# Optimization experiments

Hardware: AMD Instinct MI355X
Metric: run time of the kernel (lower is better)

The kernel has to match this reference:

```python
import jax, jax.numpy as jnp
import numpy as np

N_MEMORY = 128
INPUT_LEN = 512
OUTPUT_LEN = 256
N_FRAMES = 65536


def setup_inputs() -> dict:
    key = jax.random.key(0)
    k1, k2, k3, k4, k5 = jax.random.split(key, 5)
    return {
        "inputs": jax.random.normal(k1, (INPUT_LEN, N_FRAMES), dtype=jnp.float32),
        "W1": jax.random.normal(k2, (2 * N_MEMORY, INPUT_LEN), dtype=jnp.float32) * 0.05,
        "B1": jax.random.normal(k3, (2 * N_MEMORY, 1), dtype=jnp.float32) * 0.05,
        "W2": jax.random.normal(k4, (OUTPUT_LEN, N_MEMORY), dtype=jnp.float32) * 0.05,
        "B2": jax.random.normal(k5, (OUTPUT_LEN, 1), dtype=jnp.float32) * 0.05,
    }


def reference(inputs, W1, B1, W2, B2):
    # h: (2M, T)
    h = jax.nn.sigmoid(jnp.matmul(W1, inputs) + B1)
    M = W1.shape[0] // 2
    left, right = h[:M], h[M:]          # each (M, T)
    prod = left * right                  # gate product, (M, T)

    # Linear recurrence: u_0 = 0; u_t = prod[:, t-1] * u_{t-1} + (1 - left[:, t-1])
    # Affine pairs for t = 1..T-1, time-major: (T-1, M)
    a = prod[:, :-1].T
    b = (1.0 - left[:, :-1]).T

    def combine(c1, c2):
        a1, b1 = c1
        a2, b2 = c2
        return a1 * a2, a2 * b1 + b2

    _, bb = jax.lax.associative_scan(combine, (a, b))
    # u_0 = 0 => u_t = bb_t; prepend the zero initial state as column 0
    z = jnp.concatenate([jnp.zeros((M, 1), dtype=inputs.dtype), bb.T], axis=1)  # (M, T)

    out = 1.0 - jax.nn.sigmoid(jnp.matmul(W2, z) + B2)  # (output_len, T)
    return out
```

## Files before the change

### kernel.cpp

```cpp
#include <hip/hip_runtime.h>

typedef unsigned short u16;
typedef short bf16x8 __attribute__((ext_vector_type(8)));
typedef float f32x4 __attribute__((ext_vector_type(4)));

#define NF 65536
#define NSC 1024
#define NMAC 16

__device__ __forceinline__ float sigm(float x){ return 1.0f/(1.0f+__expf(-x)); }

__device__ __forceinline__ u16 f2bf(float f){
  union { float f; unsigned u; } v; v.f = f;
  unsigned r = (v.u + 0x7fffu + ((v.u >> 16) & 1u)) >> 16;
  return (u16)r;
}

#define AS1(p) ((const __attribute__((address_space(1))) unsigned int*)(p))
#define AS3(p) ((__attribute__((address_space(3))) unsigned int*)(p))

__global__ __launch_bounds__(256) void k_prep(const float* __restrict__ W1, const float* __restrict__ W2,
                                              u16* __restrict__ W1f, u16* __restrict__ W2f){
  int idx = blockIdx.x*256 + threadIdx.x;
  {
    int j  = idx & 7;
    int L  = (idx >> 3) & 63;
    int ks = (idx >> 9) & 1;
    int rt = (idx >> 10) & 15;
    int ck = idx >> 14;
    int row = 16*rt + (L & 15);
    int k   = ck*64 + ks*32 + ((L >> 4) << 3) + j;
    W1f[idx] = f2bf(W1[row*512 + k]);
  }
  if (idx < 32768){
    int j  = idx & 7;
    int L  = (idx >> 3) & 63;
    int ks = (idx >> 9) & 3;
    int rt = idx >> 11;
    int row = 16*rt + (L & 15);
    int m   = ks*32 + ((L >> 4) << 3) + j;
    W2f[idx] = f2bf(W2[row*128 + m]);
  }
}

__global__ __launch_bounds__(256, 4) void k_gemm1(const float* __restrict__ x,
        const u16* __restrict__ W1f, const float* __restrict__ B1,
        float* __restrict__ Aa, float* __restrict__ Bb,
        float* __restrict__ Ac, float* __restrict__ Bc){
  __shared__ __align__(16) float ls[8192];
  __shared__ __align__(16) u16  xs[4096];
  const int tid = threadIdx.x;
  const int wv = tid >> 6, L = tid & 63;
  const int q = L >> 4, ln = L & 15;
  const int g = blockIdx.x;
  const int F0 = g * 64;
  const int rt0 = 2*wv;
  const bf16x8* W1f8 = (const bf16x8*)W1f;

  f32x4 acc[4][4];
  #pragma unroll
  for (int a=0;a<4;a++)
    #pragma unroll
    for (int c=0;c<4;c++) acc[a][c] = (f32x4){0.f,0.f,0.f,0.f};

  #pragma unroll
  for (int i=0;i<4;i++){
    int seg = wv*4 + i;
    __builtin_amdgcn_global_load_lds(
      AS1(x + (size_t)(seg*4 + q)*NF + F0 + ln*4),
      AS3(ls + seg*256), 16, 0, 0);
  }

  for (int ck=0; ck<8; ++ck){
    __syncthreads();
    if (ck < 7){
      #pragma unroll
      for (int i=0;i<4;i++){
        int seg = wv*4 + i;
        __builtin_amdgcn_global_load_lds(
          AS1(x + (size_t)((ck+1)*64 + seg*4 + q)*NF + F0 + ln*4),
          AS3(ls + ((ck+1)&1)*4096 + seg*256), 16, 0, 0);
      }
    }
    bf16x8 af[2][4];
    #pragma unroll
    for (int ks=0;ks<2;ks++){
      af[ks][0] = W1f8[ck*2048 + ((rt0  )*2+ks)*64 + L];
      af[ks][1] = W1f8[ck*2048 + ((rt0+1)*2+ks)*64 + L];
      af[ks][2] = W1f8[ck*2048 + ((rt0+8)*2+ks)*64 + L];
      af[ks][3] = W1f8[ck*2048 + ((rt0+9)*2+ks)*64 + L];
    }
    {
      const float* lsb = ls + (ck&1)*4096;
      #pragma unroll
      for (int i=0;i<2;i++){
        int s    = tid + 256*i;
        int lns  = s & 15;
        int cc   = (s >> 4) & 3;
        int qs   = (s >> 6) & 3;
        int kss  = (s >> 8) & 1;
        const float* rp = lsb + (kss*32 + qs*8)*64 + cc*16 + lns;
        unsigned u[8];
        #pragma unroll
        for (int j=0;j<8;j++) u[j] = f2bf(rp[j*64]);
        uint4 pk;
        pk.x = u[0] | (u[1]<<16); pk.y = u[2] | (u[3]<<16);
        pk.z = u[4] | (u[5]<<16); pk.w = u[6] | (u[7]<<16);
        *(uint4*)(xs + ((cc*2+kss)*64 + qs*16 + lns)*8) = pk;
      }
    }
    __syncthreads();
    #pragma unroll
    for (int ks=0; ks<2; ++ks){
      #pragma unroll
      for (int c=0;c<4;c++){
        bf16x8 bf = ((const bf16x8*)xs)[(c*2+ks)*64 + L];
        acc[0][c] = __builtin_amdgcn_mfma_f32_16x16x32_bf16(af[ks][0], bf, acc[0][c], 0,0,0);
        acc[1][c] = __builtin_amdgcn_mfma_f32_16x16x32_bf16(af[ks][1], bf, acc[1][c], 0,0,0);
        acc[2][c] = __builtin_amdgcn_mfma_f32_16x16x32_bf16(af[ks][2], bf, acc[2][c], 0,0,0);
        acc[3][c] = __builtin_amdgcn_mfma_f32_16x16x32_bf16(af[ks][3], bf, acc[3][c], 0,0,0);
      }
    }
  }

  float bl[2][4], br[2][4], RA[2][4], RB[2][4];
  #pragma unroll
  for (int pr=0;pr<2;pr++){
    int mb = 32*wv + 16*pr + 4*q;
    #pragma unroll
    for (int r=0;r<4;r++){ bl[pr][r] = B1[mb+r]; br[pr][r] = B1[mb+128+r]; }
  }
  #pragma unroll
  for (int c=0;c<4;c++){
    int t = F0 + 16*c + ln;
    #pragma unroll
    for (int pr=0;pr<2;pr++){
      int mb = 32*wv + 16*pr + 4*q;
      f32x4 Lv = acc[pr][c], Rv = acc[pr+2][c];
      float a4[4], b4[4];
      #pragma unroll
      for (int r=0;r<4;r++){
        float le = sigm(Lv[r] + bl[pr][r]);
        float ri = sigm(Rv[r] + br[pr][r]);
        a4[r] = le*ri; b4[r] = 1.0f - le;
      }
      *(float4*)(Aa + (size_t)t*128 + mb) = make_float4(a4[0],a4[1],a4[2],a4[3]);
      *(float4*)(Bb + (size_t)t*128 + mb) = make_float4(b4[0],b4[1],b4[2],b4[3]);
      #pragma unroll
      for (int r=0;r<4;r++){
        float As = a4[r], Bs = b4[r];
        #pragma unroll
        for (int d=1; d<16; d<<=1){
          float Ap = __shfl_xor(As, d);
          float Bp = __shfl_xor(Bs, d);
          Bs = (ln & d) ? fmaf(As, Bp, Bs) : fmaf(Ap, Bs, Bp);
          As *= Ap;
        }
        if (c == 0){ RA[pr][r] = As; RB[pr][r] = Bs; }
        else       { RB[pr][r] = fmaf(As, RB[pr][r], Bs); RA[pr][r] *= As; }
      }
    }
  }
  if (ln == 0){
    #pragma unroll
    for (int pr=0;pr<2;pr++){
      int mb = 32*wv + 16*pr + 4*q;
      #pragma unroll
      for (int r=0;r<4;r++){
        Ac[g*128 + mb + r] = RA[pr][r];
        Bc[g*128 + mb + r] = RB[pr][r];
      }
    }
  }
}

__global__ __launch_bounds__(256) void k_scan(const float* __restrict__ Ac, const float* __restrict__ Bc,
                                              float* __restrict__ MtA, float* __restrict__ MtB){
  __shared__ float sA[2][128], sB[2][128];
  const int j = blockIdx.x;
  const int m = threadIdx.x & 127, s4 = threadIdx.x >> 7;
  const int c0 = j*64 + s4*32;
  float A = 1.f, B = 0.f;
  #pragma unroll 8
  for (int i=0;i<32;i++){
    float a = Ac[(c0+i)*128 + m], b = Bc[(c0+i)*128 + m];
    B = fmaf(a, B, b);
    A *= a;
  }
  sA[s4][m] = A; sB[s4][m] = B;
  __syncthreads();
  if (s4 == 0){
    MtA[j*128+m] = sA[1][m] * sA[0][m];
    MtB[j*128+m] = fmaf(sA[1][m], sB[0][m], sB[1][m]);
  }
}

__global__ __launch_bounds__(256, 4) void k_apply(const float* __restrict__ Aa, const float* __restrict__ Bb,
        const float* __restrict__ Ac, const float* __restrict__ Bc,
        const float* __restrict__ MtA, const float* __restrict__ MtB,
        const u16* __restrict__ W2f, const float* __restrict__ B2,
        float* __restrict__ out){
  __shared__ __align__(16) u16 zf[8192];
  __shared__ float sA[2][128], sB[2][128];
  const int tid = threadIdx.x;
  const int g = blockIdx.x, T0 = g*64;
  const int m = tid & 127, s4 = tid >> 7;

  float vg;
  {
    const int j = g >> 6, r0 = j << 6, n = g & 63;
    int c0 = r0 + s4*32, c1 = r0 + n; if (c1 > c0+32) c1 = c0+32;
    float A = 1.f, B = 0.f;
    for (int c = c0; c < c1; ++c){
      float a = Ac[c*128 + m], b = Bc[c*128 + m];
      B = fmaf(a, B, b);
      A *= a;
    }
    sA[s4][m] = A; sB[s4][m] = B;
    float v = 0.f;
    for (int jj=0; jj<j; ++jj) v = fmaf(MtA[jj*128+m], v, MtB[jj*128+m]);
    __syncthreads();
    v = fmaf(sA[0][m], v, sB[0][m]);
    v = fmaf(sA[1][m], v, sB[1][m]);
    vg = v;
    __syncthreads();
  }

  {
    const float* ap = Aa + (size_t)(T0 + s4*32)*128 + m;
    const float* bp = Bb + (size_t)(T0 + s4*32)*128 + m;
    float areg[32], breg[32];
    #pragma unroll
    for (int i=0;i<32;i++){ areg[i] = ap[(size_t)i*128]; breg[i] = bp[(size_t)i*128]; }
    float A = 1.f, Bv = 0.f;
    #pragma unroll
    for (int i=0;i<32;i++){ Bv = fmaf(areg[i], Bv, breg[i]); A *= areg[i]; }
    sA[s4][m] = A; sB[s4][m] = Bv;
    __syncthreads();
    float v = vg;
    if (s4 == 1) v = fmaf(sA[0][m], v, sB[0][m]);
    const int base_m = (m>>5)*512 + ((m>>3)&3)*128 + (m&7);
    #pragma unroll
    for (int i=0;i<32;i++){
      int t = s4*32 + i;
      zf[base_m + (t>>4)*2048 + (t&15)*8] = f2bf(v);
      v = fmaf(areg[i], v, breg[i]);
    }
  }
  __syncthreads();

  const int wv = tid >> 6, L = tid & 63;
  const int q = L >> 4, ln = L & 15;
  f32x4 acc[4][4];
  #pragma unroll
  for (int a=0;a<4;a++)
    #pragma unroll
    for (int c=0;c<4;c++) acc[a][c] = (f32x4){0.f,0.f,0.f,0.f};

  #pragma unroll
  for (int ks=0; ks<4; ++ks){
    bf16x8 af[4];
    #pragma unroll
    for (int a=0;a<4;a++) af[a] = ((const bf16x8*)W2f)[((4*wv+a)*4+ks)*64 + L];
    #pragma unroll
    for (int c=0;c<4;c++){
      bf16x8 bf = ((const bf16x8*)zf)[(c*4+ks)*64 + L];
      #pragma unroll
      for (int a=0;a<4;a++)
        acc[a][c] = __builtin_amdgcn_mfma_f32_16x16x32_bf16(af[a], bf, acc[a][c], 0,0,0);
    }
  }

  #pragma unroll
  for (int a=0;a<4;a++){
    int rowb = (4*wv+a)*16 + q*4;
    float b2[4];
    #pragma unroll
    for (int r=0;r<4;r++) b2[r] = B2[rowb+r];
    #pragma unroll
    for (int r=0;r<4;r++){
      #pragma unroll
      for (int c=0;c<4;c++)
        out[(size_t)(rowb+r)*NF + T0 + 16*c + ln] = sigm(-(acc[a][c][r] + b2[r]));
    }
  }
}

extern "C" void kernel_launch(void* const* d_in, const int* in_sizes, int n_in,
                              void* d_out, int out_size, void* d_ws, size_t ws_size,
                              hipStream_t stream) {
  const float* x  = (const float*)d_in[0];
  const float* W1 = (const float*)d_in[1];
  const float* B1 = (const float*)d_in[2];
  const float* W2 = (const float*)d_in[3];
  const float* B2 = (const float*)d_in[4];
  float* out = (float*)d_out;

  u16*   W1f = (u16*)d_ws;
  u16*   W2f = W1f + 131072;
  float* Aa  = (float*)d_ws + 81920;
  float* Bb  = Aa + (size_t)NF*128;
  float* Ac  = Bb + (size_t)NF*128;
  float* Bc  = Ac + (size_t)NSC*128;
  float* MtA = Bc + (size_t)NSC*128;
  float* MtB = MtA + (size_t)NMAC*128;

  k_prep <<<512, 256, 0, stream>>>(W1, W2, W1f, W2f);
  k_gemm1<<<NSC, 256, 0, stream>>>(x, W1f, B1, Aa, Bb, Ac, Bc);
  k_scan <<<NMAC, 256, 0, stream>>>(Ac, Bc, MtA, MtB);
  k_apply<<<NSC, 256, 0, stream>>>(Aa, Bb, Ac, Bc, MtA, MtB, W2f, B2, out);
}
```

Before: 287.2 us.

## Pack gate coefficients as bf16 pairs and stage x through registers

The per-frame recurrence coefficients (a, b) are now stored as one packed pair of bf16 values per element instead of two fp32 arrays. This halves the intermediate write and read traffic between the GEMM1 and apply kernels. The GEMM1 kernel also replaces async global-to-LDS loads with a register prefetch two chunks ahead, then stores into LDS after the conversion step. The bf16 coefficients reduce precision in a long multiplicative recurrence, and the chunk sums are computed from the rounded values so they stay consistent. The register staging adds register pressure.

```diff
diff --git a/kernel.cpp b/kernel.cpp
--- a/kernel.cpp
+++ b/kernel.cpp
@@ -15,9 +15,8 @@
   unsigned r = (v.u + 0x7fffu + ((v.u >> 16) & 1u)) >> 16;
   return (u16)r;
 }
-
-#define AS1(p) ((const __attribute__((address_space(1))) unsigned int*)(p))
-#define AS3(p) ((__attribute__((address_space(3))) unsigned int*)(p))
+__device__ __forceinline__ float bfl(unsigned p){ union{unsigned u; float f;} v; v.u = p<<16;          return v.f; }
+__device__ __forceinline__ float bfh(unsigned p){ union{unsigned u; float f;} v; v.u = p & 0xffff0000u; return v.f; }
 
 __global__ __launch_bounds__(256) void k_prep(const float* __restrict__ W1, const float* __restrict__ W2,
                                               u16* __restrict__ W1f, u16* __restrict__ W2f){
@@ -45,7 +44,7 @@
 
 __global__ __launch_bounds__(256, 4) void k_gemm1(const float* __restrict__ x,
         const u16* __restrict__ W1f, const float* __restrict__ B1,
-        float* __restrict__ Aa, float* __restrict__ Bb,
+        unsigned* __restrict__ AB,
         float* __restrict__ Ac, float* __restrict__ Bc){
   __shared__ __align__(16) float ls[8192];
   __shared__ __align__(16) u16  xs[4096];
@@ -63,25 +62,17 @@
     #pragma unroll
     for (int c=0;c<4;c++) acc[a][c] = (f32x4){0.f,0.f,0.f,0.f};
 
-  #pragma unroll
-  for (int i=0;i<4;i++){
-    int seg = wv*4 + i;
-    __builtin_amdgcn_global_load_lds(
-      AS1(x + (size_t)(seg*4 + q)*NF + F0 + ln*4),
-      AS3(ls + seg*256), 16, 0, 0);
-  }
+  #define XSRC(ck,i) ((const float4*)(x + (size_t)((ck)*64 + 16*wv + 4*(i) + q)*NF + F0 + ln*4))
+  #define LDST(buf,i) ((float4*)(ls + (buf)*4096 + (wv*4+(i))*256 + (size_t)L*4))
+  float4 vst[4];
+  #pragma unroll
+  for (int i=0;i<4;i++) vst[i] = *XSRC(0,i);
+  #pragma unroll
+  for (int i=0;i<4;i++) *LDST(0,i) = vst[i];
+  #pragma unroll
+  for (int i=0;i<4;i++) vst[i] = *XSRC(1,i);
 
   for (int ck=0; ck<8; ++ck){
-    __syncthreads();
-    if (ck < 7){
-      #pragma unroll
-      for (int i=0;i<4;i++){
-        int seg = wv*4 + i;
-        __builtin_amdgcn_global_load_lds(
-          AS1(x + (size_t)((ck+1)*64 + seg*4 + q)*NF + F0 + ln*4),
-          AS3(ls + ((ck+1)&1)*4096 + seg*256), 16, 0, 0);
-      }
-    }
     bf16x8 af[2][4];
     #pragma unroll
     for (int ks=0;ks<2;ks++){
@@ -90,6 +81,7 @@
       af[ks][2] = W1f8[ck*2048 + ((rt0+8)*2+ks)*64 + L];
       af[ks][3] = W1f8[ck*2048 + ((rt0+9)*2+ks)*64 + L];
     }
+    __syncthreads();
     {
       const float* lsb = ls + (ck&1)*4096;
       #pragma unroll
@@ -110,6 +102,14 @@
       }
     }
     __syncthreads();
+    if (ck < 7){
+      #pragma unroll
+      for (int i=0;i<4;i++) *LDST((ck+1)&1, i) = vst[i];
+      if (ck < 6){
+        #pragma unroll
+        for (int i=0;i<4;i++) vst[i] = *XSRC(ck+2, i);
+      }
+    }
     #pragma unroll
     for (int ks=0; ks<2; ++ks){
       #pragma unroll
@@ -122,6 +122,8 @@
       }
     }
   }
+  #undef XSRC
+  #undef LDST
 
   float bl[2][4], br[2][4], RA[2][4], RB[2][4];
   #pragma unroll
@@ -137,18 +139,20 @@
     for (int pr=0;pr<2;pr++){
       int mb = 32*wv + 16*pr + 4*q;
       f32x4 Lv = acc[pr][c], Rv = acc[pr+2][c];
-      float a4[4], b4[4];
+      unsigned p4[4];
+      float ar[4], brr[4];
       #pragma unroll
       for (int r=0;r<4;r++){
         float le = sigm(Lv[r] + bl[pr][r]);
         float ri = sigm(Rv[r] + br[pr][r]);
-        a4[r] = le*ri; b4[r] = 1.0f - le;
-      }
-      *(float4*)(Aa + (size_t)t*128 + mb) = make_float4(a4[0],a4[1],a4[2],a4[3]);
-      *(float4*)(Bb + (size_t)t*128 + mb) = make_float4(b4[0],b4[1],b4[2],b4[3]);
+        unsigned pa = f2bf(le*ri), pb = f2bf(1.0f - le);
+        p4[r] = pa | (pb<<16);
+        ar[r] = bfl(p4[r]); brr[r] = bfh(p4[r]);
+      }
+      *(uint4*)(AB + (size_t)t*128 + mb) = make_uint4(p4[0],p4[1],p4[2],p4[3]);
       #pragma unroll
       for (int r=0;r<4;r++){
-        float As = a4[r], Bs = b4[r];
+        float As = ar[r], Bs = brr[r];
         #pragma unroll
         for (int d=1; d<16; d<<=1){
           float Ap = __shfl_xor(As, d);
@@ -195,7 +199,7 @@
   }
 }
 
-__global__ __launch_bounds__(256, 4) void k_apply(const float* __restrict__ Aa, const float* __restrict__ Bb,
+__global__ __launch_bounds__(256, 4) void k_apply(const unsigned* __restrict__ AB,
         const float* __restrict__ Ac, const float* __restrict__ Bc,
         const float* __restrict__ MtA, const float* __restrict__ MtB,
         const u16* __restrict__ W2f, const float* __restrict__ B2,
@@ -227,14 +231,13 @@
   }
 
   {
-    const float* ap = Aa + (size_t)(T0 + s4*32)*128 + m;
-    const float* bp = Bb + (size_t)(T0 + s4*32)*128 + m;
-    float areg[32], breg[32];
-    #pragma unroll
-    for (int i=0;i<32;i++){ areg[i] = ap[(size_t)i*128]; breg[i] = bp[(size_t)i*128]; }
+    const unsigned* abp = AB + (size_t)(T0 + s4*32)*128 + m;
+    unsigned abreg[32];
+    #pragma unroll
+    for (int i=0;i<32;i++) abreg[i] = abp[(size_t)i*128];
     float A = 1.f, Bv = 0.f;
     #pragma unroll
-    for (int i=0;i<32;i++){ Bv = fmaf(areg[i], Bv, breg[i]); A *= areg[i]; }
+    for (int i=0;i<32;i++){ Bv = fmaf(bfl(abreg[i]), Bv, bfh(abreg[i])); A *= bfl(abreg[i]); }
     sA[s4][m] = A; sB[s4][m] = Bv;
     __syncthreads();
     float v = vg;
@@ -244,7 +247,7 @@
     for (int i=0;i<32;i++){
       int t = s4*32 + i;
       zf[base_m + (t>>4)*2048 + (t&15)*8] = f2bf(v);
-      v = fmaf(areg[i], v, breg[i]);
+      v = fmaf(bfl(abreg[i]), v, bfh(abreg[i]));
     }
   }
   __syncthreads();
@@ -296,17 +299,16 @@
   const float* B2 = (const float*)d_in[4];
   float* out = (float*)d_out;
 
-  u16*   W1f = (u16*)d_ws;
-  u16*   W2f = W1f + 131072;
-  float* Aa  = (float*)d_ws + 81920;
-  float* Bb  = Aa + (size_t)NF*128;
-  float* Ac  = Bb + (size_t)NF*128;
-  float* Bc  = Ac + (size_t)NSC*128;
-  float* MtA = Bc + (size_t)NSC*128;
-  float* MtB = MtA + (size_t)NMAC*128;
+  u16*      W1f = (u16*)d_ws;
+  u16*      W2f = W1f + 131072;
+  unsigned* AB  = (unsigned*)d_ws + 81920;
+  float*    Ac  = (float*)(AB + (size_t)NF*128);
+  float*    Bc  = Ac + (size_t)NSC*128;
+  float*    MtA = Bc + (size_t)NSC*128;
+  float*    MtB = MtA + (size_t)NMAC*128;
 
   k_prep <<<512, 256, 0, stream>>>(W1, W2, W1f, W2f);
-  k_gemm1<<<NSC, 256, 0, stream>>>(x, W1f, B1, Aa, Bb, Ac, Bc);
+  k_gemm1<<<NSC, 256, 0, stream>>>(x, W1f, B1, AB, Ac, Bc);
   k_scan <<<NMAC, 256, 0, stream>>>(Ac, Bc, MtA, MtB);
-  k_apply<<<NSC, 256, 0, stream>>>(Aa, Bb, Ac, Bc, MtA, MtB, W2f, B2, out);
-}
+  k_apply<<<NSC, 256, 0, stream>>>(AB, Ac, Bc, MtA, MtB, W2f, B2, out);
+}
```

Measured after the change: 305.2 us. 6.3% more time.
